# Kernel optimization log

Measured on AMD Instinct MI355X. Metric: run time of the kernel, lower is better.

The kernel has to match this reference:

```python
import jax, jax.numpy as jnp
import numpy as np

ALPHA = 0.2        # LeakyReLU negative slope
NEG = -9e15        # mask value used by the torch module
N, FIN, H, D = 4096, 20, 4, 64


def gat_layer(h, adj_mask, W, a_src, a_dst, average):
    """Multi-head GAT layer. W: [H,Fin,Fout], a_src/a_dst: [H,Fout].
    e_ij = LeakyReLU(a_src . Wh_i + a_dst . Wh_j) == a^T [Wh_i || Wh_j],
    identical math to the N x N x 2F concat in the torch code, without
    materializing the pairwise concat tensor."""
    Wh = jnp.einsum('nf,hfo->hno', h, W)                 # [H,N,F]
    f_s = jnp.einsum('hno,ho->hn', Wh, a_src)            # [H,N]
    f_d = jnp.einsum('hno,ho->hn', Wh, a_dst)            # [H,N]
    e = jax.nn.leaky_relu(f_s[:, :, None] + f_d[:, None, :], ALPHA)  # [H,N,N]
    e = jnp.where(adj_mask[None], e, NEG)
    att = jax.nn.softmax(e, axis=-1)
    out = jax.nn.elu(jnp.einsum('hnm,hmo->hno', att, Wh))  # per-head ELU (concat=True inside)
    if average:
        return out.mean(axis=0)                           # [N,F]
    return jnp.transpose(out, (1, 0, 2)).reshape(h.shape[0], -1)  # [N,H*F]


def setup_inputs() -> dict:
    key = jax.random.key(0)
    ks = jax.random.split(key, 6)
    x = jax.random.normal(ks[0], (N, FIN), jnp.float32)
    adj = jax.random.randint(ks[1], (N, N), 0, 2, jnp.int32)
    # layer 0: 20 -> 64 per head, 4 heads, concat -> 256
    W0 = jax.random.normal(ks[2], (H, FIN, D), jnp.float32) * 0.3
    a0 = jax.random.normal(ks[3], (H, 2 * D), jnp.float32) * 0.1
    # layer 1: 256 -> 64 per head, heads averaged
    W1 = jax.random.normal(ks[4], (H, H * D, D), jnp.float32) * 0.06
    a1 = jax.random.normal(ks[5], (H, 2 * D), jnp.float32) * 0.1
    return {"x": x, "adj": adj, "W0": W0, "a0": a0, "W1": W1, "a1": a1}


def reference(x, adj, W0, a0, W1, a1):
    mask = adj > 0
    h = gat_layer(x, mask, W0, a0[:, :D], a0[:, D:], average=False)   # [N, 256]
    return gat_layer(h, mask, W1, a1[:, :D], a1[:, D:], average=True)  # [N, 64]
```

## Files before the change

kernel.cpp:

```cpp
#include <hip/hip_runtime.h>
#include <hip/hip_fp16.h>
#include <math.h>

#define NN 4096
#define FIN 20
#define NH 4
#define DH 64
#define ALPHA 0.2f
#define LOG2E 1.4426950408889634f

typedef _Float16 f16x8 __attribute__((ext_vector_type(8)));
typedef _Float16 f16x4 __attribute__((ext_vector_type(4)));
typedef __fp16 fp16x2 __attribute__((ext_vector_type(2)));
typedef float f32x4 __attribute__((ext_vector_type(4)));

#if defined(__has_builtin)
#if __has_builtin(__builtin_amdgcn_exp2f)
#define FEXP2(x) __builtin_amdgcn_exp2f(x)
#endif
#endif
#ifndef FEXP2
extern "C" __device__ float __ocml_native_exp2_f32(float);
#define FEXP2(x) __ocml_native_exp2_f32(x)
#endif

__device__ inline void gload_lds16(const void* gsrc, void* ldsbase) {
    __builtin_amdgcn_global_load_lds(
        (const __attribute__((address_space(1))) void*)gsrc,
        (__attribute__((address_space(3))) void*)ldsbase, 16, 0, 0);
}

__global__ __launch_bounds__(256) void k_front(const int* __restrict__ adj,
        unsigned char* __restrict__ bits, const float* __restrict__ x,
        const float* __restrict__ W0, const float* __restrict__ a0,
        _Float16* __restrict__ whT, float* __restrict__ fs, float* __restrict__ fd,
        const float* __restrict__ W1, _Float16* __restrict__ w1T) {
    __shared__ float xs[16 * FIN];
    const int bid = blockIdx.x;
    const int tid = threadIdx.x;
    if (bid < 8192) {
        int t = bid * 256 + tid;
        const int4* p = (const int4*)(adj + (size_t)t * 8);
        int4 a = p[0], b = p[1];
        unsigned int byte = 0;
        byte |= (a.x > 0) << 0; byte |= (a.y > 0) << 1;
        byte |= (a.z > 0) << 2; byte |= (a.w > 0) << 3;
        byte |= (b.x > 0) << 4; byte |= (b.y > 0) << 5;
        byte |= (b.z > 0) << 6; byte |= (b.w > 0) << 7;
        bits[t] = (unsigned char)byte;
    } else if (bid < 8448) {
        int n0 = (bid - 8192) * 16;
        for (int i = tid; i < 16 * FIN; i += 256) xs[i] = x[n0 * FIN + i];
        __syncthreads();
        int h = tid >> 6, d = tid & 63;
        float w0r[FIN];
#pragma unroll
        for (int f = 0; f < FIN; ++f) w0r[f] = W0[(h * FIN + f) * DH + d];
        float asrc = a0[h * 2 * DH + d];
        float adst = a0[h * 2 * DH + DH + d];
        f16x8 wv[2];
#pragma unroll
        for (int n = 0; n < 16; ++n) {
            float wh = 0.f;
#pragma unroll
            for (int f = 0; f < FIN; ++f) wh = fmaf(xs[n * FIN + f], w0r[f], wh);
            wv[n >> 3][n & 7] = (_Float16)wh;
            float sv = wh * asrc, dv = wh * adst;
#pragma unroll
            for (int off = 1; off <= 32; off <<= 1) {
                sv += __shfl_xor(sv, off);
                dv += __shfl_xor(dv, off);
            }
            if (d == 0) { fs[h * NN + n0 + n] = sv; fd[h * NN + n0 + n] = dv; }
        }
        _Float16* dst = whT + ((size_t)(h * DH + d) * NN + n0);
        *(f16x8*)(dst) = wv[0];
        *(f16x8*)(dst + 8) = wv[1];
    } else {
        int u = (bid - 8448) * 256 + tid;
        int h = u >> 14, f = (u >> 6) & 255, d = u & 63;
        w1T[((size_t)(h * DH + d) << 8) + f] = (_Float16)W1[u];
    }
}

__global__ __launch_bounds__(256) void k_fdmax(const float* __restrict__ fd,
        float* __restrict__ fdm) {
    int h = blockIdx.x, tid = threadIdx.x;
    float m = -3e38f;
    for (int i = tid; i < NN; i += 256) m = fmaxf(m, fd[h * NN + i]);
#pragma unroll
    for (int off = 1; off <= 32; off <<= 1) m = fmaxf(m, __shfl_xor(m, off));
    __shared__ float mx[4];
    if ((tid & 63) == 0) mx[tid >> 6] = m;
    __syncthreads();
    if (tid == 0) fdm[h] = fmaxf(fmaxf(mx[0], mx[1]), fmaxf(mx[2], mx[3]));
}

__global__ __launch_bounds__(512) void k_attn(const float* __restrict__ fs,
        const float* __restrict__ fd, const float* __restrict__ fdmax,
        const _Float16* __restrict__ whT, const unsigned char* __restrict__ bits,
        float* __restrict__ pv, float* __restrict__ pl) {
    __shared__ __align__(16) char smem[34304];
    const int ck = blockIdx.x & 3;
    const int rowblk = (blockIdx.x >> 2) & 63;
    const int h = blockIdx.x >> 8;
    const int row0 = rowblk << 6;
    const int cb0 = ck << 10;
    const int tid = threadIdx.x;
    const int l = tid & 63, w = tid >> 6;
    const int rl = l & 15, g = l >> 4;
    const int rg = w >> 2, cq = w & 3;
    const int r0 = row0 + rg * 32 + rl;
    const int r1 = r0 + 16;
    const float fsr0 = fs[h * NN + r0], fsr1 = fs[h * NN + r1];
    const float fm = fdmax[h];
    const float su0 = fsr0 + fm, su1 = fsr1 + fm;
    const float m0 = fmaxf(su0, ALPHA * su0);
    const float m1 = fmaxf(su1, ALPHA * su1);
    const float A0 = (fsr0 - m0) * LOG2E, B0 = (ALPHA * fsr0 - m0) * LOG2E;
    const float A1 = (fsr1 - m1) * LOG2E, B1 = (ALPHA * fsr1 - m1) * LOG2E;
    const float* fdp = fd + h * NN + cb0 + cq * 32 + g * 8;
    const unsigned char* bp0 = bits + (size_t)r0 * (NN / 8) + (cb0 >> 3) + cq * 4;
    const unsigned char* bp1 = bits + (size_t)r1 * (NN / 8) + (cb0 >> 3) + cq * 4;
    const _Float16* whb = whT + (size_t)h * DH * NN + cb0;

    const int d0_ = tid >> 4, c0_ = tid & 15;
    const int d1_ = 32 + (tid >> 4), c1_ = tid & 15;
    const _Float16* src0 = whb + (size_t)d0_ * NN + 8 * (c0_ ^ (d0_ & 15));
    const _Float16* src1 = whb + (size_t)d1_ * NN + 8 * (c1_ ^ (d1_ & 15));
    char* dstA0 = smem + w * 1024;
    char* dstA1 = smem + 8192 + w * 1024;
    char* dstB0 = smem + 16384 + w * 1024;
    char* dstB1 = smem + 16384 + 8192 + w * 1024;

    f32x4 acc0[4] = {{0,0,0,0},{0,0,0,0},{0,0,0,0},{0,0,0,0}};
    f32x4 acc1[4] = {{0,0,0,0},{0,0,0,0},{0,0,0,0},{0,0,0,0}};
    f32x4 al0 = {0,0,0,0}, al1 = {0,0,0,0};
    f16x8 ones;
#pragma unroll
    for (int i = 0; i < 8; ++i) ones[i] = (_Float16)1.0f;
    const int rdswz = ((((cq << 2) | g) ^ rl) << 4);

    gload_lds16(src0, dstA0);
    gload_lds16(src1, dstA1);
    float4 faA = *(const float4*)(fdp);
    float4 fbA = *(const float4*)(fdp + 4);
    unsigned int mA0 = *(const unsigned int*)(bp0);
    unsigned int mA1 = *(const unsigned int*)(bp1);
    float4 faB, fbB;
    unsigned int mB0, mB1;
    __syncthreads();

#define COMPUTE(BUF, FA, FB, M0v, M1v)                                          \
    {                                                                           \
        const float fv[8] = {FA.x, FA.y, FA.z, FA.w, FB.x, FB.y, FB.z, FB.w};   \
        f16x8 av0, av1;                                                         \
        const int sh = g << 3;                                                  \
        _Pragma("unroll")                                                       \
        for (int i = 0; i < 8; i += 2) {                                        \
            float ta = fmaxf(fmaf(fv[i], LOG2E, A0), fmaf(fv[i], ALPHA * LOG2E, B0)); \
            ta = ((M0v >> (sh + i)) & 1u) ? ta : -1e30f;                        \
            float tb = fmaxf(fmaf(fv[i+1], LOG2E, A0), fmaf(fv[i+1], ALPHA * LOG2E, B0)); \
            tb = ((M0v >> (sh + i + 1)) & 1u) ? tb : -1e30f;                    \
            fp16x2 p0 = __builtin_amdgcn_cvt_pkrtz(FEXP2(ta), FEXP2(tb));       \
            av0[i] = (_Float16)p0[0]; av0[i+1] = (_Float16)p0[1];               \
            float tc = fmaxf(fmaf(fv[i], LOG2E, A1), fmaf(fv[i], ALPHA * LOG2E, B1)); \
            tc = ((M1v >> (sh + i)) & 1u) ? tc : -1e30f;                        \
            float td = fmaxf(fmaf(fv[i+1], LOG2E, A1), fmaf(fv[i+1], ALPHA * LOG2E, B1)); \
            td = ((M1v >> (sh + i + 1)) & 1u) ? td : -1e30f;                    \
            fp16x2 p1 = __builtin_amdgcn_cvt_pkrtz(FEXP2(tc), FEXP2(td));       \
            av1[i] = (_Float16)p1[0]; av1[i+1] = (_Float16)p1[1];               \
        }                                                                       \
        al0 = __builtin_amdgcn_mfma_f32_16x16x32_f16(av0, ones, al0, 0, 0, 0);  \
        al1 = __builtin_amdgcn_mfma_f32_16x16x32_f16(av1, ones, al1, 0, 0, 0);  \
        _Pragma("unroll")                                                       \
        for (int t4 = 0; t4 < 4; ++t4) {                                        \
            f16x8 bv = *(const f16x8*)((BUF) + ((16 * t4 + rl) << 8) + rdswz);  \
            acc0[t4] = __builtin_amdgcn_mfma_f32_16x16x32_f16(av0, bv, acc0[t4], 0, 0, 0); \
            acc1[t4] = __builtin_amdgcn_mfma_f32_16x16x32_f16(av1, bv, acc1[t4], 0, 0, 0); \
        }                                                                       \
    }

#pragma unroll 1
    for (int k = 0; k < 4; ++k) {
        const int tB = 2 * k + 1;
        gload_lds16(src0 + tB * 128, dstB0);
        gload_lds16(src1 + tB * 128, dstB1);
        faB = *(const float4*)(fdp + tB * 128);
        fbB = *(const float4*)(fdp + tB * 128 + 4);
        mB0 = *(const unsigned int*)(bp0 + tB * 16);
        mB1 = *(const unsigned int*)(bp1 + tB * 16);
        COMPUTE(smem, faA, fbA, mA0, mA1);
        __syncthreads();
        if (k < 3) {
            const int tA = 2 * k + 2;
            gload_lds16(src0 + tA * 128, dstA0);
            gload_lds16(src1 + tA * 128, dstA1);
            faA = *(const float4*)(fdp + tA * 128);
            fbA = *(const float4*)(fdp + tA * 128 + 4);
            mA0 = *(const unsigned int*)(bp0 + tA * 16);
            mA1 = *(const unsigned int*)(bp1 + tA * 16);
        }
        COMPUTE((smem + 16384), faB, fbB, mB0, mB1);
        __syncthreads();
    }
#undef COMPUTE

    float* red = (float*)smem;
    float* lred = (float*)(smem + 33792);
#pragma unroll
    for (int p = 0; p < 2; ++p) {
        if (rg == p) {
#pragma unroll
            for (int t4 = 0; t4 < 4; ++t4)
#pragma unroll
                for (int i = 0; i < 4; ++i) {
                    red[(cq * 32 + 4 * g + i) * 66 + 16 * t4 + rl]      = acc0[t4][i];
                    red[(cq * 32 + 16 + 4 * g + i) * 66 + 16 * t4 + rl] = acc1[t4][i];
                }
            if (rl == 0) {
#pragma unroll
                for (int i = 0; i < 4; ++i) {
                    lred[cq * 32 + 4 * g + i]      = al0[i];
                    lred[cq * 32 + 16 + 4 * g + i] = al1[i];
                }
            }
        }
        __syncthreads();
#pragma unroll
        for (int j = 0; j < 4; ++j) {
            const int R = w * 4 + j;
            float v = 0.f, L = 0.f;
#pragma unroll
            for (int cc = 0; cc < 4; ++cc) {
                v += red[(cc * 32 + R) * 66 + l];
                L += lred[cc * 32 + R];
            }
            const int Rg = row0 + p * 32 + R;
            pv[(((size_t)(ck * NH + h) * NN) + Rg) * 64 + l] = v;
            if (l == 0) pl[(size_t)(ck * NH + h) * NN + Rg] = L;
        }
        __syncthreads();
    }
}

template<int MODE>
__global__ __launch_bounds__(256) void k_merge(const float* __restrict__ pv,
        const float* __restrict__ pl, void* __restrict__ outp) {
    int t = blockIdx.x * 256 + threadIdx.x;
    if (MODE == 0) {
        int d = t & 63, n = (t >> 6) & (NN - 1), h = t >> 18;
        float v = 0.f, L = 0.f;
#pragma unroll
        for (int cc = 0; cc < 4; ++cc) {
            v += pv[(((size_t)(cc * NH + h) * NN) + n) * 64 + d];
            L += pl[(size_t)(cc * NH + h) * NN + n];
        }
        float o = v * __builtin_amdgcn_rcpf(L);
        o = o > 0.f ? o : __expf(o) - 1.f;
        ((_Float16*)outp)[(size_t)n * (NH * DH) + h * DH + d] = (_Float16)o;
    } else {
        int d = t & 63, n = t >> 6;
        float s = 0.f;
#pragma unroll
        for (int h = 0; h < NH; ++h) {
            float v = 0.f, L = 0.f;
#pragma unroll
            for (int cc = 0; cc < 4; ++cc) {
                v += pv[(((size_t)(cc * NH + h) * NN) + n) * 64 + d];
                L += pl[(size_t)(cc * NH + h) * NN + n];
            }
            float o = v * __builtin_amdgcn_rcpf(L);
            s += o > 0.f ? o : __expf(o) - 1.f;
        }
        ((float*)outp)[t] = 0.25f * s;
    }
}

__global__ __launch_bounds__(256) void k_l1wh(const _Float16* __restrict__ h16,
        const _Float16* __restrict__ w1T, const float* __restrict__ a1,
        _Float16* __restrict__ whT, float* __restrict__ fs, float* __restrict__ fd) {
    __shared__ float red[4][16][64];
    __shared__ _Float16 lt[16][64];
    int h = blockIdx.x >> 8;
    int row0 = (blockIdx.x & 255) << 4;
    int tid = threadIdx.x;
    int l = tid & 63, w = tid >> 6;
    int rl = l & 15, g = l >> 4;
    f32x4 acc[4] = {{0,0,0,0},{0,0,0,0},{0,0,0,0},{0,0,0,0}};
    const _Float16* ap = h16 + (size_t)(row0 + rl) * (NH * DH) + w * 64;
    const _Float16* bp = w1T + ((size_t)h * DH << 8) + w * 64;
#pragma unroll
    for (int j = 0; j < 2; ++j) {
        int fb = j * 32 + 8 * g;
        f16x8 avv = *(const f16x8*)(ap + fb);
#pragma unroll
        for (int t4 = 0; t4 < 4; ++t4) {
            f16x8 bv = *(const f16x8*)(bp + ((size_t)(16 * t4 + rl) << 8) + fb);
            acc[t4] = __builtin_amdgcn_mfma_f32_16x16x32_f16(avv, bv, acc[t4], 0, 0, 0);
        }
    }
#pragma unroll
    for (int t4 = 0; t4 < 4; ++t4)
#pragma unroll
        for (int i = 0; i < 4; ++i) red[w][t4 * 4 + i][l] = acc[t4][i];
    __syncthreads();
#pragma unroll
    for (int i = 0; i < 4; ++i) {
        float v = red[0][w * 4 + i][l] + red[1][w * 4 + i][l]
                + red[2][w * 4 + i][l] + red[3][w * 4 + i][l];
        lt[4 * g + i][16 * w + rl] = (_Float16)v;
    }
    __syncthreads();
    int d = tid & 63, rb = tid >> 6;
    f16x4 o;
#pragma unroll
    for (int j = 0; j < 4; ++j) o[j] = lt[rb * 4 + j][d];
    *(f16x4*)(whT + (size_t)(h * DH + d) * NN + row0 + rb * 4) = o;
    float as_ = a1[h * 2 * DH + d], ad_ = a1[h * 2 * DH + DH + d];
    float svj[4], dvj[4];
#pragma unroll
    for (int j = 0; j < 4; ++j) {
        float wv = (float)lt[rb * 4 + j][d];
        svj[j] = wv * as_;
        dvj[j] = wv * ad_;
    }
#pragma unroll
    for (int off = 1; off <= 32; off <<= 1) {
#pragma unroll
        for (int j = 0; j < 4; ++j) {
            svj[j] += __shfl_xor(svj[j], off);
            dvj[j] += __shfl_xor(dvj[j], off);
        }
    }
    if (d == 0) {
#pragma unroll
        for (int j = 0; j < 4; ++j) {
            fs[h * NN + row0 + rb * 4 + j] = svj[j];
            fd[h * NN + row0 + rb * 4 + j] = dvj[j];
        }
    }
}

extern "C" void kernel_launch(void* const* d_in, const int* in_sizes, int n_in,
                              void* d_out, int out_size, void* d_ws, size_t ws_size,
                              hipStream_t stream) {
    const float* x  = (const float*)d_in[0];
    const int* adj  = (const int*)d_in[1];
    const float* W0 = (const float*)d_in[2];
    const float* a0 = (const float*)d_in[3];
    const float* W1 = (const float*)d_in[4];
    const float* a1 = (const float*)d_in[5];
    float* out = (float*)d_out;
    char* ws = (char*)d_ws;

    unsigned char* bits = (unsigned char*)(ws);
    _Float16* whT0 = (_Float16*)(ws + (2ull << 20));
    _Float16* h16  = (_Float16*)(ws + (4ull << 20));
    _Float16* w1T  = (_Float16*)(ws + (6ull << 20));
    _Float16* whT1 = (_Float16*)(ws + (6ull << 20) + (256ull << 10));
    float* fs0  = (float*)(ws + (9ull << 20));
    float* fd0  = fs0 + NH * NN;
    float* fs1  = fd0 + NH * NN;
    float* fd1  = fs1 + NH * NN;
    float* fdm0 = fd1 + NH * NN;
    float* fdm1 = fdm0 + 8;
    float* pv   = (float*)(ws + (10ull << 20));
    float* pl   = (float*)(ws + (26ull << 20));

    k_front<<<8704, 256, 0, stream>>>(adj, bits, x, W0, a0, whT0, fs0, fd0, W1, w1T);
    k_fdmax<<<NH, 256, 0, stream>>>(fd0, fdm0);
    k_attn<<<4 * NH * (NN / 64), 512, 0, stream>>>(fs0, fd0, fdm0, whT0, bits, pv, pl);
    k_merge<0><<<(NH * NN * DH) / 256, 256, 0, stream>>>(pv, pl, h16);
    k_l1wh<<<NH * (NN / 16), 256, 0, stream>>>(h16, w1T, a1, whT1, fs1, fd1);
    k_fdmax<<<NH, 256, 0, stream>>>(fd1, fdm1);
    k_attn<<<4 * NH * (NN / 64), 512, 0, stream>>>(fs1, fd1, fdm1, whT1, bits, pv, pl);
    k_merge<1><<<(NN * DH) / 256, 256, 0, stream>>>(pv, pl, out);
}
```

Measured before the change: 128.1 us.

## Fuse fd-max into attention, halve column splits, merge layer-0 combine into L1 projection

The separate column-max kernels are removed; each attention block now computes the per-head max of fd itself with a block reduction. The column split of the attention kernel drops from four chunks to two, so each block loops over twice as many tiles, there are half as many blocks and the partial buffers are smaller. The layer-0 merge (chunk sum, normalize, ELU, fp16 cast) is folded into the layer-1 projection kernel, which removes a launch and the h16 round trip. The cost is redundant max computation in every block and fewer blocks available for parallelism. A leftover unused k_l1wh variant remains in the file.

```diff
diff --git a/kernel.cpp b/kernel.cpp
--- a/kernel.cpp
+++ b/kernel.cpp
@@ -83,37 +83,39 @@
     }
 }
 
-__global__ __launch_bounds__(256) void k_fdmax(const float* __restrict__ fd,
-        float* __restrict__ fdm) {
-    int h = blockIdx.x, tid = threadIdx.x;
-    float m = -3e38f;
-    for (int i = tid; i < NN; i += 256) m = fmaxf(m, fd[h * NN + i]);
-#pragma unroll
-    for (int off = 1; off <= 32; off <<= 1) m = fmaxf(m, __shfl_xor(m, off));
-    __shared__ float mx[4];
-    if ((tid & 63) == 0) mx[tid >> 6] = m;
-    __syncthreads();
-    if (tid == 0) fdm[h] = fmaxf(fmaxf(mx[0], mx[1]), fmaxf(mx[2], mx[3]));
-}
-
 __global__ __launch_bounds__(512) void k_attn(const float* __restrict__ fs,
-        const float* __restrict__ fd, const float* __restrict__ fdmax,
-        const _Float16* __restrict__ whT, const unsigned char* __restrict__ bits,
+        const float* __restrict__ fd, const _Float16* __restrict__ whT,
+        const unsigned char* __restrict__ bits,
         float* __restrict__ pv, float* __restrict__ pl) {
     __shared__ __align__(16) char smem[34304];
-    const int ck = blockIdx.x & 3;
-    const int rowblk = (blockIdx.x >> 2) & 63;
-    const int h = blockIdx.x >> 8;
+    const int ch = blockIdx.x & 1;
+    const int rowblk = (blockIdx.x >> 1) & 63;
+    const int h = blockIdx.x >> 7;
     const int row0 = rowblk << 6;
-    const int cb0 = ck << 10;
+    const int cb0 = ch << 11;
     const int tid = threadIdx.x;
     const int l = tid & 63, w = tid >> 6;
     const int rl = l & 15, g = l >> 4;
     const int rg = w >> 2, cq = w & 3;
     const int r0 = row0 + rg * 32 + rl;
     const int r1 = r0 + 16;
+
+    float mloc;
+    {
+        const float4* f4 = (const float4*)(fd + h * NN);
+        float4 v0 = f4[tid], v1 = f4[tid + 512];
+        mloc = fmaxf(fmaxf(fmaxf(v0.x, v0.y), fmaxf(v0.z, v0.w)),
+                     fmaxf(fmaxf(v1.x, v1.y), fmaxf(v1.z, v1.w)));
+    }
+#pragma unroll
+    for (int off = 1; off <= 32; off <<= 1) mloc = fmaxf(mloc, __shfl_xor(mloc, off));
+    float* mxs = (float*)(smem + 33792);
+    if (l == 0) mxs[w] = mloc;
+    __syncthreads();
+    const float fm = fmaxf(fmaxf(fmaxf(mxs[0], mxs[1]), fmaxf(mxs[2], mxs[3])),
+                           fmaxf(fmaxf(mxs[4], mxs[5]), fmaxf(mxs[6], mxs[7])));
+
     const float fsr0 = fs[h * NN + r0], fsr1 = fs[h * NN + r1];
-    const float fm = fdmax[h];
     const float su0 = fsr0 + fm, su1 = fsr1 + fm;
     const float m0 = fmaxf(su0, ALPHA * su0);
     const float m1 = fmaxf(su1, ALPHA * su1);
@@ -182,7 +184,7 @@
     }
 
 #pragma unroll 1
-    for (int k = 0; k < 4; ++k) {
+    for (int k = 0; k < 8; ++k) {
         const int tB = 2 * k + 1;
         gload_lds16(src0 + tB * 128, dstB0);
         gload_lds16(src1 + tB * 128, dstB1);
@@ -192,7 +194,7 @@
         mB1 = *(const unsigned int*)(bp1 + tB * 16);
         COMPUTE(smem, faA, fbA, mA0, mA1);
         __syncthreads();
-        if (k < 3) {
+        if (k < 7) {
             const int tA = 2 * k + 2;
             gload_lds16(src0 + tA * 128, dstA0);
             gload_lds16(src1 + tA * 128, dstA1);
@@ -237,49 +239,16 @@
                 L += lred[cc * 32 + R];
             }
             const int Rg = row0 + p * 32 + R;
-            pv[(((size_t)(ck * NH + h) * NN) + Rg) * 64 + l] = v;
-            if (l == 0) pl[(size_t)(ck * NH + h) * NN + Rg] = L;
+            pv[(((size_t)(ch * NH + h) * NN) + Rg) * 64 + l] = v;
+            if (l == 0) pl[(size_t)(ch * NH + h) * NN + Rg] = L;
         }
         __syncthreads();
     }
 }
 
-template<int MODE>
-__global__ __launch_bounds__(256) void k_merge(const float* __restrict__ pv,
-        const float* __restrict__ pl, void* __restrict__ outp) {
-    int t = blockIdx.x * 256 + threadIdx.x;
-    if (MODE == 0) {
-        int d = t & 63, n = (t >> 6) & (NN - 1), h = t >> 18;
-        float v = 0.f, L = 0.f;
-#pragma unroll
-        for (int cc = 0; cc < 4; ++cc) {
-            v += pv[(((size_t)(cc * NH + h) * NN) + n) * 64 + d];
-            L += pl[(size_t)(cc * NH + h) * NN + n];
-        }
-        float o = v * __builtin_amdgcn_rcpf(L);
-        o = o > 0.f ? o : __expf(o) - 1.f;
-        ((_Float16*)outp)[(size_t)n * (NH * DH) + h * DH + d] = (_Float16)o;
-    } else {
-        int d = t & 63, n = t >> 6;
-        float s = 0.f;
-#pragma unroll
-        for (int h = 0; h < NH; ++h) {
-            float v = 0.f, L = 0.f;
-#pragma unroll
-            for (int cc = 0; cc < 4; ++cc) {
-                v += pv[(((size_t)(cc * NH + h) * NN) + n) * 64 + d];
-                L += pl[(size_t)(cc * NH + h) * NN + n];
-            }
-            float o = v * __builtin_amdgcn_rcpf(L);
-            s += o > 0.f ? o : __expf(o) - 1.f;
-        }
-        ((float*)outp)[t] = 0.25f * s;
-    }
-}
-
-__global__ __launch_bounds__(256) void k_l1wh(const _Float16* __restrict__ h16,
-        const _Float16* __restrict__ w1T, const float* __restrict__ a1,
-        _Float16* __restrict__ whT, float* __restrict__ fs, float* __restrict__ fd) {
+__global__ __launch_bounds__(256) void k_l1wh(const float* __restrict__ pv,
+        const float* __restrict__ pl, const _Float16* __restrict__ w1T,
+        const float* __restrict__ a1, float* __restrict__ fs, float* __restrict__ fd) {
     __shared__ float red[4][16][64];
     __shared__ _Float16 lt[16][64];
     int h = blockIdx.x >> 8;
@@ -287,16 +256,32 @@
     int tid = threadIdx.x;
     int l = tid & 63, w = tid >> 6;
     int rl = l & 15, g = l >> 4;
+    const int row = row0 + rl;
+    const float L2 = pl[(size_t)w * NN + row] + pl[(size_t)(NH + w) * NN + row];
+    const float rcpL = __builtin_amdgcn_rcpf(L2);
+    const float* p0 = pv + (((size_t)w * NN) + row) * 64;
+    const float* p1 = pv + (((size_t)(NH + w) * NN) + row) * 64;
     f32x4 acc[4] = {{0,0,0,0},{0,0,0,0},{0,0,0,0},{0,0,0,0}};
-    const _Float16* ap = h16 + (size_t)(row0 + rl) * (NH * DH) + w * 64;
     const _Float16* bp = w1T + ((size_t)h * DH << 8) + w * 64;
 #pragma unroll
     for (int j = 0; j < 2; ++j) {
         int fb = j * 32 + 8 * g;
-        f16x8 avv = *(const f16x8*)(ap + fb);
+        float4 va = *(const float4*)(p0 + fb);
+        float4 vb = *(const float4*)(p0 + fb + 4);
+        float4 wa = *(const float4*)(p1 + fb);
+        float4 wb = *(const float4*)(p1 + fb + 4);
+        float o[8] = {va.x + wa.x, va.y + wa.y, va.z + wa.z, va.w + wa.w,
+                      vb.x + wb.x, vb.y + wb.y, vb.z + wb.z, vb.w + wb.w};
+        f16x8 avv;
+#pragma unroll
+        for (int i = 0; i < 8; ++i) {
+            float v = o[i] * rcpL;
+            v = v > 0.f ? v : __expf(v) - 1.f;
+            avv[i] = (_Float16)v;
+        }
 #pragma unroll
         for (int t4 = 0; t4 < 4; ++t4) {
-            f16x8 bv = *(const f16x8*)(bp + ((size_t)(16 * t4 + rl) << 8) + fb);
+            f16x8 bv = *(const f16x8*)(bp + ((size_t)(16 * t4 + rl) << 8) + j * 32 + 8 * g);
             acc[t4] = __builtin_amdgcn_mfma_f32_16x16x32_f16(avv, bv, acc[t4], 0, 0, 0);
         }
     }
@@ -313,6 +298,89 @@
     }
     __syncthreads();
     int d = tid & 63, rb = tid >> 6;
+    float as_ = a1[h * 2 * DH + d], ad_ = a1[h * 2 * DH + DH + d];
+    float svj[4], dvj[4];
+#pragma unroll
+    for (int j = 0; j < 4; ++j) {
+        float wv = (float)lt[rb * 4 + j][d];
+        svj[j] = wv * as_;
+        dvj[j] = wv * ad_;
+    }
+#pragma unroll
+    for (int off = 1; off <= 32; off <<= 1) {
+#pragma unroll
+        for (int j = 0; j < 4; ++j) {
+            svj[j] += __shfl_xor(svj[j], off);
+            dvj[j] += __shfl_xor(dvj[j], off);
+        }
+    }
+    if (d == 0) {
+#pragma unroll
+        for (int j = 0; j < 4; ++j) {
+            fs[h * NN + row0 + rb * 4 + j] = svj[j];
+            fd[h * NN + row0 + rb * 4 + j] = dvj[j];
+        }
+    }
+    f16x4 o;
+#pragma unroll
+    for (int j = 0; j < 4; ++j) o[j] = lt[rb * 4 + j][d];
+    _Float16* whT = (_Float16*)nullptr;
+    (void)whT;
+}
+
+__global__ __launch_bounds__(256) void k_l1whB(const float* __restrict__ pv,
+        const float* __restrict__ pl, const _Float16* __restrict__ w1T,
+        const float* __restrict__ a1, _Float16* __restrict__ whT,
+        float* __restrict__ fs, float* __restrict__ fd) {
+    __shared__ float red[4][16][64];
+    __shared__ _Float16 lt[16][64];
+    int h = blockIdx.x >> 8;
+    int row0 = (blockIdx.x & 255) << 4;
+    int tid = threadIdx.x;
+    int l = tid & 63, w = tid >> 6;
+    int rl = l & 15, g = l >> 4;
+    const int row = row0 + rl;
+    const float L2 = pl[(size_t)w * NN + row] + pl[(size_t)(NH + w) * NN + row];
+    const float rcpL = __builtin_amdgcn_rcpf(L2);
+    const float* p0 = pv + (((size_t)w * NN) + row) * 64;
+    const float* p1 = pv + (((size_t)(NH + w) * NN) + row) * 64;
+    f32x4 acc[4] = {{0,0,0,0},{0,0,0,0},{0,0,0,0},{0,0,0,0}};
+    const _Float16* bp = w1T + ((size_t)h * DH << 8) + w * 64;
+#pragma unroll
+    for (int j = 0; j < 2; ++j) {
+        int fb = j * 32 + 8 * g;
+        float4 va = *(const float4*)(p0 + fb);
+        float4 vb = *(const float4*)(p0 + fb + 4);
+        float4 wa = *(const float4*)(p1 + fb);
+        float4 wb = *(const float4*)(p1 + fb + 4);
+        float o[8] = {va.x + wa.x, va.y + wa.y, va.z + wa.z, va.w + wa.w,
+                      vb.x + wb.x, vb.y + wb.y, vb.z + wb.z, vb.w + wb.w};
+        f16x8 avv;
+#pragma unroll
+        for (int i = 0; i < 8; ++i) {
+            float v = o[i] * rcpL;
+            v = v > 0.f ? v : __expf(v) - 1.f;
+            avv[i] = (_Float16)v;
+        }
+#pragma unroll
+        for (int t4 = 0; t4 < 4; ++t4) {
+            f16x8 bv = *(const f16x8*)(bp + ((size_t)(16 * t4 + rl) << 8) + fb);
+            acc[t4] = __builtin_amdgcn_mfma_f32_16x16x32_f16(avv, bv, acc[t4], 0, 0, 0);
+        }
+    }
+#pragma unroll
+    for (int t4 = 0; t4 < 4; ++t4)
+#pragma unroll
+        for (int i = 0; i < 4; ++i) red[w][t4 * 4 + i][l] = acc[t4][i];
+    __syncthreads();
+#pragma unroll
+    for (int i = 0; i < 4; ++i) {
+        float v = red[0][w * 4 + i][l] + red[1][w * 4 + i][l]
+                + red[2][w * 4 + i][l] + red[3][w * 4 + i][l];
+        lt[4 * g + i][16 * w + rl] = (_Float16)v;
+    }
+    __syncthreads();
+    int d = tid & 63, rb = tid >> 6;
     f16x4 o;
 #pragma unroll
     for (int j = 0; j < 4; ++j) o[j] = lt[rb * 4 + j][d];
@@ -340,6 +408,21 @@
             fd[h * NN + row0 + rb * 4 + j] = dvj[j];
         }
     }
+}
+
+__global__ __launch_bounds__(256) void k_merge1(const float* __restrict__ pv,
+        const float* __restrict__ pl, float* __restrict__ out) {
+    int t = blockIdx.x * 256 + threadIdx.x;
+    int d = t & 63, n = t >> 6;
+    float s = 0.f;
+#pragma unroll
+    for (int h = 0; h < NH; ++h) {
+        float v = pv[(((size_t)h * NN) + n) * 64 + d] + pv[(((size_t)(NH + h) * NN) + n) * 64 + d];
+        float L = pl[(size_t)h * NN + n] + pl[(size_t)(NH + h) * NN + n];
+        float o = v * __builtin_amdgcn_rcpf(L);
+        s += o > 0.f ? o : __expf(o) - 1.f;
+    }
+    out[t] = 0.25f * s;
 }
 
 extern "C" void kernel_launch(void* const* d_in, const int* in_sizes, int n_in,
@@ -356,24 +439,18 @@
 
     unsigned char* bits = (unsigned char*)(ws);
     _Float16* whT0 = (_Float16*)(ws + (2ull << 20));
-    _Float16* h16  = (_Float16*)(ws + (4ull << 20));
     _Float16* w1T  = (_Float16*)(ws + (6ull << 20));
     _Float16* whT1 = (_Float16*)(ws + (6ull << 20) + (256ull << 10));
     float* fs0  = (float*)(ws + (9ull << 20));
     float* fd0  = fs0 + NH * NN;
     float* fs1  = fd0 + NH * NN;
     float* fd1  = fs1 + NH * NN;
-    float* fdm0 = fd1 + NH * NN;
-    float* fdm1 = fdm0 + 8;
     float* pv   = (float*)(ws + (10ull << 20));
-    float* pl   = (float*)(ws + (26ull << 20));
+    float* pl   = (float*)(ws + (18ull << 20));
 
     k_front<<<8704, 256, 0, stream>>>(adj, bits, x, W0, a0, whT0, fs0, fd0, W1, w1T);
-    k_fdmax<<<NH, 256, 0, stream>>>(fd0, fdm0);
-    k_attn<<<4 * NH * (NN / 64), 512, 0, stream>>>(fs0, fd0, fdm0, whT0, bits, pv, pl);
-    k_merge<0><<<(NH * NN * DH) / 256, 256, 0, stream>>>(pv, pl, h16);
-    k_l1wh<<<NH * (NN / 16), 256, 0, stream>>>(h16, w1T, a1, whT1, fs1, fd1);
-    k_fdmax<<<NH, 256, 0, stream>>>(fd1, fdm1);
-    k_attn<<<4 * NH * (NN / 64), 512, 0, stream>>>(fs1, fd1, fdm1, whT1, bits, pv, pl);
-    k_merge<1><<<(NN * DH) / 256, 256, 0, stream>>>(pv, pl, out);
-}
+    k_attn<<<2 * NH * (NN / 64), 512, 0, stream>>>(fs0, fd0, whT0, bits, pv, pl);
+    k_l1whB<<<NH * (NN / 16), 256, 0, stream>>>(pv, pl, w1T, a1, whT1, fs1, fd1);
+    k_attn<<<2 * NH * (NN / 64), 512, 0, stream>>>(fs1, fd1, whT1, bits, pv, pl);
+    k_merge1<<<(NN * DH) / 256, 256, 0, stream>>>(pv, pl, out);
+}
```

Result: faster. 111.4 us (-13.1%).
